# Optimization experiments

Hardware: AMD Instinct MI355X
Metric: run time of the kernel (lower is better)

## Reference

```python
import jax, jax.numpy as jnp
import numpy as np

RES = 14
KEY_DIM = 32
NUM_HEADS = 12
ATTN_RATIO = 4
DIM = 384
VAL_ATTN_DIM = ATTN_RATIO * KEY_DIM * NUM_HEADS  # 1536
QKV_DIM = VAL_ATTN_DIM + 2 * KEY_DIM * NUM_HEADS  # 2304
BN_EPS = 1e-5


def _bias_idxs():
    # torch.meshgrid default is 'ij'
    gy, gx = jnp.meshgrid(jnp.arange(RES), jnp.arange(RES), indexing='ij')
    pos = jnp.stack([gy.reshape(-1), gx.reshape(-1)])           # [2, N]
    rel = jnp.abs(pos[:, :, None] - pos[:, None, :])            # [2, N, N]
    return rel[0] * RES + rel[1]                                # [N, N] int


def _linear_bn(x, w, gamma, beta, mean, var):
    # bias-free Linear (torch weight layout [out,in]) + BatchNorm1d (eval)
    y = x @ w.T
    inv = gamma / jnp.sqrt(var + BN_EPS)
    return y * inv + (beta - mean * inv)


def setup_inputs() -> dict:
    key = jax.random.key(0)
    ks = jax.random.split(key, 12)
    B, N = 128, RES * RES
    f = jax.random.normal
    return {
        'x': f(ks[0], (B, N, DIM), jnp.float32),
        'qkv_w': f(ks[1], (QKV_DIM, DIM), jnp.float32) * 0.02,
        'qkv_gamma': f(ks[2], (QKV_DIM,), jnp.float32) * 0.1 + 1.0,
        'qkv_beta': f(ks[3], (QKV_DIM,), jnp.float32) * 0.1,
        'qkv_mean': f(ks[4], (QKV_DIM,), jnp.float32) * 0.1,
        'qkv_var': jax.random.uniform(ks[5], (QKV_DIM,), jnp.float32, 0.5, 1.5),
        'attn_biases': f(ks[6], (NUM_HEADS, RES * RES), jnp.float32) * 0.1,
        'proj_w': f(ks[7], (DIM, VAL_ATTN_DIM), jnp.float32) * 0.02,
        'proj_gamma': f(ks[8], (DIM,), jnp.float32) * 0.1 + 1.0,
        'proj_beta': f(ks[9], (DIM,), jnp.float32) * 0.1,
        'proj_mean': f(ks[10], (DIM,), jnp.float32) * 0.1,
        'proj_var': jax.random.uniform(ks[11], (DIM,), jnp.float32, 0.5, 1.5),
    }


def reference(x, qkv_w, qkv_gamma, qkv_beta, qkv_mean, qkv_var,
              attn_biases, proj_w, proj_gamma, proj_beta, proj_mean, proj_var):
    B, N, _ = x.shape
    scale = KEY_DIM ** -0.5
    qkv = _linear_bn(x, qkv_w, qkv_gamma, qkv_beta, qkv_mean, qkv_var)
    qkv = qkv.reshape(B, N, NUM_HEADS, -1)
    q = qkv[..., :KEY_DIM]                       # [B,N,H,dk]
    k = qkv[..., KEY_DIM:2 * KEY_DIM]            # [B,N,H,dk]
    v = qkv[..., 2 * KEY_DIM:]                   # [B,N,H,dv]
    bias = attn_biases[:, _bias_idxs()]          # [H,N,N]
    attn = jnp.einsum('bnhd,bmhd->bhnm', q, k) * scale + bias[None]
    attn = jax.nn.softmax(attn, axis=-1)
    out = jnp.einsum('bhnm,bmhd->bnhd', attn, v).reshape(B, N, VAL_ATTN_DIM)
    out = jax.nn.silu(out)
    return _linear_bn(out, proj_w, proj_gamma, proj_beta, proj_mean, proj_var)
```

## Files before the change

### kernel.cpp

```cpp
#include <hip/hip_runtime.h>
#include <cstdint>

#define NQ 196
#define DIMX 384
#define QKVD 2304
#define VAD 1536
#define NHD 12
#define MTOT 25088

#define KSTR 40
#define VSTR 232
#define TSTR 140

typedef unsigned int u32;
typedef unsigned short u16;
typedef __bf16 bf16_t;
typedef bf16_t bf16x8 __attribute__((ext_vector_type(8)));
typedef float f32x4 __attribute__((ext_vector_type(4)));

__device__ inline u16 f2b(float f) {
  u32 u = __float_as_uint(f);
  u32 r = (u + 0x7fffu + ((u >> 16) & 1u)) >> 16;
  return (u16)r;
}
__device__ inline float b2f(u16 u) { return __uint_as_float(((u32)u) << 16); }
__device__ inline int iabs(int v) { return v < 0 ? -v : v; }

__device__ inline void gld_lds16(const void* g, void* l) {
  __builtin_amdgcn_global_load_lds((__attribute__((address_space(1))) void*)g,
                                   (__attribute__((address_space(3))) void*)l,
                                   16, 0, 0);
}


__global__ void cvt_kernel(const float* __restrict__ in, u16* __restrict__ out, int n4) {
  int i = blockIdx.x * 256 + threadIdx.x;
  if (i >= n4) return;
  float4 v = ((const float4*)in)[i];
  ushort4 o;
  o.x = f2b(v.x); o.y = f2b(v.y); o.z = f2b(v.z); o.w = f2b(v.w);
  ((ushort4*)out)[i] = o;
}

__global__ void cvt_wqkv(const float* __restrict__ in, u16* __restrict__ out) {
  int i = blockIdx.x * 256 + threadIdx.x;
  if (i >= QKVD * DIMX / 4) return;
  const int newc = i / (DIMX / 4);
  const int kc = (i - newc * (DIMX / 4)) * 4;
  int oldc;
  if (newc < 384)      { int h = newc >> 5;              oldc = h * 192 + (newc & 31); }
  else if (newc < 768) { int t = newc - 384; int h = t >> 5; oldc = h * 192 + 32 + (t & 31); }
  else                 { int t = newc - 768; int h = t >> 7; oldc = h * 192 + 64 + (t & 127); }
  float4 v = *(const float4*)(in + (size_t)oldc * DIMX + kc);
  ushort4 o;
  o.x = f2b(v.x); o.y = f2b(v.y); o.z = f2b(v.z); o.w = f2b(v.w);
  *(ushort4*)(out + (size_t)newc * DIMX + kc) = o;
}

__global__ void bn_tab(const float* __restrict__ g, const float* __restrict__ be,
                       const float* __restrict__ mn, const float* __restrict__ vr,
                       float* __restrict__ inv, float* __restrict__ off, int n) {
  int i = blockIdx.x * 256 + threadIdx.x;
  if (i >= n) return;
  float iv = g[i] * rsqrtf(vr[i] + 1e-5f);
  inv[i] = iv;
  off[i] = be[i] - mn[i] * iv;
}

__global__ void bn_tab_qkv(const float* __restrict__ g, const float* __restrict__ be,
                           const float* __restrict__ mn, const float* __restrict__ vr,
                           float* __restrict__ inv, float* __restrict__ off) {
  int i = blockIdx.x * 256 + threadIdx.x;
  if (i >= QKVD) return;
  const int h = i / 192, r = i - h * 192;
  const int newc = (r < 32) ? h * 32 + r
                 : (r < 64) ? 384 + h * 32 + (r - 32)
                            : 768 + h * 128 + (r - 64);
  float iv = g[i] * rsqrtf(vr[i] + 1e-5f);
  inv[newc] = iv;
  off[newc] = be[i] - mn[i] * iv;
}

__global__ void bias_tiles(const float* __restrict__ biases, float* __restrict__ bt) {
  const int blk = blockIdx.x;
  const int h = blk / 169, r2 = blk - h * 169;
  const int rt = r2 / 13, t = r2 - rt * 13;
  const int lane = threadIdx.x;
  const int fr = lane & 15, fj = lane >> 4;
  const int m = t * 16 + fr;
  const bool mv = m < NQ;
  const int ym = mv ? m / 14 : 0;
  const int xm = mv ? (m - ym * 14) : 0;
  f32x4 v;
#pragma unroll
  for (int rg = 0; rg < 4; rg++) {
    int n = rt * 16 + fj * 4 + rg;
    n = n > 195 ? 195 : n;
    const int yn = n / 14, xn = n - yn * 14;
    v[rg] = mv ? biases[h * NQ + iabs(yn - ym) * 14 + iabs(xn - xm)] : -1e30f;
  }
  *((f32x4*)bt + (size_t)blk * 64 + lane) = v;
}


template <int MODE>
__global__ __launch_bounds__(256) void gemm_bt(
    const u16* __restrict__ A, const u16* __restrict__ B, int K,
    const float* __restrict__ inv, const float* __restrict__ off,
    u16* __restrict__ Qb, u16* __restrict__ Kb, u16* __restrict__ Vt,
    float* __restrict__ out) {
  constexpr int LDSU = (MODE == 0) ? 128 * TSTR : 8192;
  __shared__ __align__(16) u16 lds[LDSU];
  u16* As = lds;
  u16* Bs = lds + 4096;
  const int tid = threadIdx.x;
  const int wid = tid >> 6, lane = tid & 63;
  const int wm = wid & 1, wn = wid >> 1;
  const int fr = lane & 15, fk = (lane >> 4) << 3;
  const u16* Ab = A + (size_t)(blockIdx.y * 128) * K;
  const u16* Bb = B + (size_t)(blockIdx.x * 128) * K;
  const int c0 = (wid << 6) | lane;
  const int r0 = c0 >> 2, kc0 = (c0 & 3) << 3;
  const int c1 = c0 + 256;
  const int r1 = c1 >> 2, kc1 = (c1 & 3) << 3;

  f32x4 acc[4][4] = {};

  for (int k0 = 0; k0 < K; k0 += 32) {
    gld_lds16(Ab + (size_t)r0 * K + (k0 + kc0), &As[wid << 9]);
    gld_lds16(Ab + (size_t)r1 * K + (k0 + kc1), &As[2048 + (wid << 9)]);
    gld_lds16(Bb + (size_t)r0 * K + (k0 + kc0), &Bs[wid << 9]);
    gld_lds16(Bb + (size_t)r1 * K + (k0 + kc1), &Bs[2048 + (wid << 9)]);
    __syncthreads();
    bf16x8 av[4], bv[4];
#pragma unroll
    for (int t = 0; t < 4; t++)
      av[t] = *(const bf16x8*)&As[(wm * 64 + t * 16 + fr) * 32 + fk];
#pragma unroll
    for (int t = 0; t < 4; t++)
      bv[t] = *(const bf16x8*)&Bs[(wn * 64 + t * 16 + fr) * 32 + fk];
#pragma unroll
    for (int mt = 0; mt < 4; mt++)
#pragma unroll
      for (int nt = 0; nt < 4; nt++)
        acc[mt][nt] = __builtin_amdgcn_mfma_f32_16x16x32_bf16(av[mt], bv[nt], acc[mt][nt], 0, 0, 0);
    __syncthreads();
  }

  const int lrow0 = wm * 64 + ((lane >> 4) << 2);
  const int lcol0 = wn * 64 + fr;

  if (MODE == 0) {
    const int bx = blockIdx.x, by = blockIdx.y;
    const bool isV = bx >= 6;
#pragma unroll
    for (int nt = 0; nt < 4; nt++) {
      const int lc = lcol0 + nt * 16;
      const int gc = bx * 128 + lc;
      const float iv = inv[gc], of = off[gc];
#pragma unroll
      for (int mt = 0; mt < 4; mt++)
#pragma unroll
        for (int rg = 0; rg < 4; rg++) {
          const int lr = lrow0 + mt * 16 + rg;
          const u16 us = f2b(acc[mt][nt][rg] * iv + of);
          if (isV) lds[lc * TSTR + lr] = us;
          else     lds[lr * TSTR + lc] = us;
        }
    }
    __syncthreads();
    if (!isV) {
      u16* dstB = (bx < 3) ? Qb : Kb;
      const int h0 = (bx < 3 ? bx : bx - 3) * 4;
#pragma unroll
      for (int it = 0; it < 8; it++) {
        const int idx = it * 256 + tid;
        const int ch = idx & 3, hl = (idx >> 2) & 3, row = idx >> 4;
        const int rowg = by * 128 + row;
        const int b = rowg / 196, n = rowg - b * 196;
        const size_t bh = (size_t)(b * NHD + h0 + hl);
        const u16* src = &lds[row * TSTR + hl * 32 + ch * 8];
        uint2 a0 = *(const uint2*)src;
        uint2 a1 = *(const uint2*)(src + 4);
        *(uint4*)(dstB + (bh * NQ + n) * 32 + ch * 8) = make_uint4(a0.x, a0.y, a1.x, a1.y);
      }
    } else {
      const int h = bx - 6;
#pragma unroll
      for (int it = 0; it < 16; it++) {
        const int idx = it * 256 + tid;
        const int nk = idx & 31, col = idx >> 5;
        const int rowg = by * 128 + nk * 4;
        const int b = rowg / 196, n = rowg - b * 196;
        uint2 v = *(const uint2*)&lds[col * TSTR + nk * 4];
        *(uint2*)(Vt + ((size_t)(b * NHD + h) * 128 + col) * NQ + n) = v;
      }
    }
  } else {
    const int colb = blockIdx.x * 128 + lcol0;
    const int rowb = blockIdx.y * 128 + lrow0;
#pragma unroll
    for (int nt = 0; nt < 4; nt++) {
      const int col = colb + nt * 16;
      const float iv = inv[col], of = off[col];
#pragma unroll
      for (int mt = 0; mt < 4; mt++)
#pragma unroll
        for (int rg = 0; rg < 4; rg++) {
          const int row = rowb + mt * 16 + rg;
          out[(size_t)row * DIMX + col] = acc[mt][nt][rg] * iv + of;
        }
    }
  }
}


__global__ __launch_bounds__(512) void attn_kernel(
    const u16* __restrict__ Qg, const u16* __restrict__ Kg,
    const u16* __restrict__ Vtg, const float* __restrict__ biasT,
    u16* __restrict__ AO) {
  __shared__ __align__(16) u16 Ks[208 * KSTR];
  __shared__ __align__(16) u16 Vs[128 * VSTR];
  __shared__ __align__(16) u16 Ps[8][16 * VSTR];

  const int tid = threadIdx.x, wid = tid >> 6, lane = tid & 63;
  const int fr = lane & 15, fj = lane >> 4, fk = fj << 3;
  const int bh = blockIdx.x, b = bh / NHD, h = bh - b * NHD;
  const float scale = 0.17677669529663687f;

  for (int i = tid; i < NQ * 4; i += 512) {
    const int m = i >> 2, kc = (i & 3) << 3;
    uint4 v = *(const uint4*)(Kg + ((size_t)bh * NQ + m) * 32 + kc);
    *(uint4*)&Ks[m * KSTR + kc] = v;
  }
  if (tid < 240) ((u32*)Ks)[3920 + tid] = 0u;
  {
    const u32* src = (const u32*)(Vtg + (size_t)bh * 128 * NQ);
    u32* dst = (u32*)Vs;
    const int c1 = lane + 64;
    const int rEnd = wid * 16 + 16;
    for (int r = wid * 16; r < rEnd; r++) {
      const u32* srow = src + r * 98;
      u32* drow = dst + r * (VSTR / 2);
      drow[lane] = srow[lane];
      if (c1 < VSTR / 2) drow[c1] = (c1 < 98) ? srow[c1] : 0u;
    }
  }
  {
    const int row = lane >> 2, c = 208 + (lane & 3) * 4;
    *(uint2*)&Ps[wid][row * VSTR + c] = make_uint2(0u, 0u);
  }
  __syncthreads();

  for (int rt = wid; rt < 13; rt += 8) {
    int qrow = rt * 16 + fr; qrow = qrow > 195 ? 195 : qrow;
    const bf16x8 qf = *(const bf16x8*)(Qg + ((size_t)bh * NQ + qrow) * 32 + fk);

    f32x4 s[13];
#pragma unroll
    for (int t = 0; t < 13; t++) {
      const bf16x8 kf = *(const bf16x8*)&Ks[(t * 16 + fr) * KSTR + fk];
      f32x4 z = {0.f, 0.f, 0.f, 0.f};
      s[t] = __builtin_amdgcn_mfma_f32_16x16x32_bf16(qf, kf, z, 0, 0, 0);
    }

    const f32x4* btp = (const f32x4*)biasT + ((size_t)(h * 169 + rt * 13) * 64 + lane);
    f32x4 bt[13];
#pragma unroll
    for (int t = 0; t < 13; t++) bt[t] = btp[t * 64];
#pragma unroll
    for (int t = 0; t < 13; t++)
#pragma unroll
      for (int rg = 0; rg < 4; rg++)
        s[t][rg] = s[t][rg] * scale + bt[t][rg];

    float rinv[4];
#pragma unroll
    for (int rg = 0; rg < 4; rg++) {
      float mx = s[0][rg];
#pragma unroll
      for (int t = 1; t < 13; t++) mx = fmaxf(mx, s[t][rg]);
      mx = fmaxf(mx, __shfl_xor(mx, 1));
      mx = fmaxf(mx, __shfl_xor(mx, 2));
      mx = fmaxf(mx, __shfl_xor(mx, 4));
      mx = fmaxf(mx, __shfl_xor(mx, 8));
      float ls = 0.f;
#pragma unroll
      for (int t = 0; t < 13; t++) {
        const float e = __expf(s[t][rg] - mx);
        s[t][rg] = e;
        ls += e;
      }
      ls += __shfl_xor(ls, 1);
      ls += __shfl_xor(ls, 2);
      ls += __shfl_xor(ls, 4);
      ls += __shfl_xor(ls, 8);
      rinv[rg] = 1.f / ls;
    }
#pragma unroll
    for (int t = 0; t < 13; t++)
#pragma unroll
      for (int rg = 0; rg < 4; rg++)
        Ps[wid][(fj * 4 + rg) * VSTR + t * 16 + fr] = f2b(s[t][rg]);
    __threadfence_block();

    f32x4 o[8] = {};
#pragma unroll
    for (int kc = 0; kc < 7; kc++) {
      const bf16x8 pf = *(const bf16x8*)&Ps[wid][fr * VSTR + kc * 32 + fk];
#pragma unroll
      for (int dt = 0; dt < 8; dt++) {
        const bf16x8 vf = *(const bf16x8*)&Vs[(dt * 16 + fr) * VSTR + kc * 32 + fk];
        o[dt] = __builtin_amdgcn_mfma_f32_16x16x32_bf16(pf, vf, o[dt], 0, 0, 0);
      }
    }
#pragma unroll
    for (int rg = 0; rg < 4; rg++) {
      const float rv = rinv[rg];
#pragma unroll
      for (int dt = 0; dt < 8; dt++) {
        float x = o[dt][rg] * rv;
        x = x / (1.f + __expf(-x));
        Ps[wid][(fj * 4 + rg) * VSTR + dt * 16 + fr] = f2b(x);
      }
    }
    __threadfence_block();
#pragma unroll
    for (int it = 0; it < 4; it++) {
      const int idx = it * 64 + lane;
      const int row = idx >> 4, dc = idx & 15;
      const int n = rt * 16 + row;
      if (n < NQ) {
        uint4 v = *(const uint4*)&Ps[wid][row * VSTR + dc * 8];
        *(uint4*)(AO + ((size_t)(b * NQ + n)) * VAD + h * 128 + dc * 8) = v;
      }
    }
    __threadfence_block();
  }
}


extern "C" void kernel_launch(void* const* d_in, const int* in_sizes, int n_in,
                              void* d_out, int out_size, void* d_ws, size_t ws_size,
                              hipStream_t stream) {
  const float* x          = (const float*)d_in[0];
  const float* qkv_w      = (const float*)d_in[1];
  const float* qkv_gamma  = (const float*)d_in[2];
  const float* qkv_beta   = (const float*)d_in[3];
  const float* qkv_mean   = (const float*)d_in[4];
  const float* qkv_var    = (const float*)d_in[5];
  const float* attn_bias  = (const float*)d_in[6];
  const float* proj_w     = (const float*)d_in[7];
  const float* proj_gamma = (const float*)d_in[8];
  const float* proj_beta  = (const float*)d_in[9];
  const float* proj_mean  = (const float*)d_in[10];
  const float* proj_var   = (const float*)d_in[11];

  const size_t szXB    = (size_t)MTOT * DIMX * 2;
  const size_t szQKVW  = (size_t)QKVD * DIMX * 2;
  const size_t szPROJW = (size_t)DIMX * VAD * 2;
  const size_t szQK    = (size_t)128 * NHD * NQ * 32 * 2;
  const size_t szV     = (size_t)128 * NHD * 128 * NQ * 2;
  const size_t szAO    = (size_t)MTOT * VAD * 2;
  const size_t szBT    = (size_t)NHD * 169 * 64 * 4 * 4;
  const size_t szX     = (szXB + szQKVW > szAO) ? (szXB + szQKVW) : szAO;

  char* w = (char*)d_ws;
  u16* projwb = (u16*)w; w += szPROJW;
  float* inv1 = (float*)w; w += QKVD * 4;
  float* off1 = (float*)w; w += QKVD * 4;
  float* inv2 = (float*)w; w += DIMX * 4;
  float* off2 = (float*)w; w += DIMX * 4;
  float* biasT = (float*)w; w += szBT;
  u16* Qb = (u16*)w; w += szQK;
  u16* Kb = (u16*)w; w += szQK;
  u16* Vt = (u16*)w; w += szV;
  char* regionX = w; w += szX;
  u16* xb    = (u16*)regionX;
  u16* qkvwb = (u16*)(regionX + szXB);
  u16* AO    = (u16*)regionX;

  if ((size_t)(w - (char*)d_ws) > ws_size) return;

  cvt_kernel<<<MTOT * DIMX / 4 / 256, 256, 0, stream>>>(x, xb, MTOT * DIMX / 4);
  cvt_wqkv<<<(QKVD * DIMX / 4 + 255) / 256, 256, 0, stream>>>(qkv_w, qkvwb);
  cvt_kernel<<<DIMX * VAD / 4 / 256, 256, 0, stream>>>(proj_w, projwb, DIMX * VAD / 4);
  bn_tab_qkv<<<(QKVD + 255) / 256, 256, 0, stream>>>(qkv_gamma, qkv_beta, qkv_mean, qkv_var, inv1, off1);
  bn_tab<<<(DIMX + 255) / 256, 256, 0, stream>>>(proj_gamma, proj_beta, proj_mean, proj_var, inv2, off2, DIMX);
  bias_tiles<<<NHD * 169, 64, 0, stream>>>(attn_bias, biasT);

  gemm_bt<0><<<dim3(QKVD / 128, MTOT / 128), 256, 0, stream>>>(
      xb, qkvwb, DIMX, inv1, off1, Qb, Kb, Vt, nullptr);
  attn_kernel<<<128 * NHD, 512, 0, stream>>>(Qb, Kb, Vt, biasT, AO);
  gemm_bt<1><<<dim3(DIMX / 128, MTOT / 128), 256, 0, stream>>>(
      AO, projwb, VAD, inv2, off2, nullptr, nullptr, nullptr, (float*)d_out);
}
```

Baseline: 429.3 us.

## Read V fragments directly from global memory instead of staging through LDS

The attention kernel drops the per-block LDS copy of transposed V and loads the MFMA V fragments straight from global memory. To keep those loads 16-byte aligned, the V workspace is re-laid out with a padded row stride of 200. The kernel also gets a min-blocks occupancy hint, and the bias load is folded into the scaling loop to cut register pressure. This removes a large LDS allocation and the staging pass, at the cost of every wave re-reading V through the cache. Reads now run past column 196 into padding and the next row's data instead of a zeroed LDS pad, and the tighter register budget may cause spills.

```diff
diff --git a/kernel.cpp b/kernel.cpp
--- a/kernel.cpp
+++ b/kernel.cpp
@@ -11,6 +11,7 @@
 #define KSTR 40
 #define VSTR 232
 #define TSTR 140
+#define VGSTR 200
 
 typedef unsigned int u32;
 typedef unsigned short u16;
@@ -193,7 +194,7 @@
         const int rowg = by * 128 + nk * 4;
         const int b = rowg / 196, n = rowg - b * 196;
         uint2 v = *(const uint2*)&lds[col * TSTR + nk * 4];
-        *(uint2*)(Vt + ((size_t)(b * NHD + h) * 128 + col) * NQ + n) = v;
+        *(uint2*)(Vt + ((size_t)(b * NHD + h) * 128 + col) * VGSTR + n) = v;
       }
     }
   } else {
@@ -215,12 +216,11 @@
 }
 
 
-__global__ __launch_bounds__(512) void attn_kernel(
+__global__ __launch_bounds__(512, 4) void attn_kernel(
     const u16* __restrict__ Qg, const u16* __restrict__ Kg,
     const u16* __restrict__ Vtg, const float* __restrict__ biasT,
     u16* __restrict__ AO) {
   __shared__ __align__(16) u16 Ks[208 * KSTR];
-  __shared__ __align__(16) u16 Vs[128 * VSTR];
   __shared__ __align__(16) u16 Ps[8][16 * VSTR];
 
   const int tid = threadIdx.x, wid = tid >> 6, lane = tid & 63;
@@ -235,22 +235,12 @@
   }
   if (tid < 240) ((u32*)Ks)[3920 + tid] = 0u;
   {
-    const u32* src = (const u32*)(Vtg + (size_t)bh * 128 * NQ);
-    u32* dst = (u32*)Vs;
-    const int c1 = lane + 64;
-    const int rEnd = wid * 16 + 16;
-    for (int r = wid * 16; r < rEnd; r++) {
-      const u32* srow = src + r * 98;
-      u32* drow = dst + r * (VSTR / 2);
-      drow[lane] = srow[lane];
-      if (c1 < VSTR / 2) drow[c1] = (c1 < 98) ? srow[c1] : 0u;
-    }
-  }
-  {
     const int row = lane >> 2, c = 208 + (lane & 3) * 4;
     *(uint2*)&Ps[wid][row * VSTR + c] = make_uint2(0u, 0u);
   }
   __syncthreads();
+
+  const u16* Vb = Vtg + (size_t)bh * 128 * VGSTR;
 
   for (int rt = wid; rt < 13; rt += 8) {
     int qrow = rt * 16 + fr; qrow = qrow > 195 ? 195 : qrow;
@@ -265,14 +255,13 @@
     }
 
     const f32x4* btp = (const f32x4*)biasT + ((size_t)(h * 169 + rt * 13) * 64 + lane);
-    f32x4 bt[13];
-#pragma unroll
-    for (int t = 0; t < 13; t++) bt[t] = btp[t * 64];
-#pragma unroll
-    for (int t = 0; t < 13; t++)
+#pragma unroll
+    for (int t = 0; t < 13; t++) {
+      const f32x4 bt = btp[t * 64];
 #pragma unroll
       for (int rg = 0; rg < 4; rg++)
-        s[t][rg] = s[t][rg] * scale + bt[t][rg];
+        s[t][rg] = s[t][rg] * scale + bt[rg];
+    }
 
     float rinv[4];
 #pragma unroll
@@ -310,7 +299,7 @@
       const bf16x8 pf = *(const bf16x8*)&Ps[wid][fr * VSTR + kc * 32 + fk];
 #pragma unroll
       for (int dt = 0; dt < 8; dt++) {
-        const bf16x8 vf = *(const bf16x8*)&Vs[(dt * 16 + fr) * VSTR + kc * 32 + fk];
+        const bf16x8 vf = *(const bf16x8*)(Vb + (dt * 16 + fr) * VGSTR + kc * 32 + fk);
         o[dt] = __builtin_amdgcn_mfma_f32_16x16x32_bf16(pf, vf, o[dt], 0, 0, 0);
       }
     }
@@ -360,7 +349,7 @@
   const size_t szQKVW  = (size_t)QKVD * DIMX * 2;
   const size_t szPROJW = (size_t)DIMX * VAD * 2;
   const size_t szQK    = (size_t)128 * NHD * NQ * 32 * 2;
-  const size_t szV     = (size_t)128 * NHD * 128 * NQ * 2;
+  const size_t szV     = (size_t)128 * NHD * 128 * VGSTR * 2;
   const size_t szAO    = (size_t)MTOT * VAD * 2;
   const size_t szBT    = (size_t)NHD * 169 * 64 * 4 * 4;
   const size_t szX     = (szXB + szQKVW > szAO) ? (szXB + szQKVW) : szAO;
```

Measured after the change: 725.3 us. 69.0% more time.
